# Optimization experiments

Hardware: AMD Instinct MI355X
Metric: run time of the kernel (lower is better)

## Reference

```python
import jax, jax.numpy as jnp
import numpy as np

CX, CY, FX, FY = 334.081, 169.808, 460.585, 460.268
EPS = 1e-07
T_ITER = 1000
MIN_POINTS = 5000
H, W, B = 360, 640, 2


def _point_cloud(depth_img):
    # depth_img: [C,H,W]; channel 2 if C==3 else channel 0
    depth = depth_img[2] if depth_img.shape[0] == 3 else depth_img[0]
    rows, cols = depth.shape
    c = jnp.arange(cols, dtype=depth.dtype)[None, :]
    r = jnp.arange(rows, dtype=depth.dtype)[:, None]
    valid = (depth > 0) & (depth < 65535)
    nanv = jnp.float32(jnp.nan)
    z = jnp.where(valid, depth / 1000.0, nanv)
    x = jnp.where(valid, z * (c - CX) / FX, nanv)
    y = jnp.where(valid, z * (r - CY) / FY, nanv)
    pcd = jnp.stack([x.ravel(), y.ravel(), z.ravel()], axis=1)  # [N,3]
    return pcd, valid.ravel()


def setup_inputs() -> dict:
    key = jax.random.key(0)
    k1, k2 = jax.random.split(key)
    fake = jax.random.uniform(k1, (B, 1, H, W), dtype=jnp.float32)
    real = jax.random.uniform(k2, (B, 1, H, W), dtype=jnp.float32)
    return {"fake": fake, "real": real, "epoch": 5, "show_image": 0}


def _forward(fake, real, epoch):
    real_pcd, vr = _point_cloud(real[0])
    fake_pcd, vf = _point_cloud(fake[0])
    real_pcd = real_pcd * 1000.0
    fake_pcd = fake_pcd * 1000.0
    # pcd[pcd==0] = eps  (NaN==0 is False, NaNs preserved)
    real_pcd = jnp.where(real_pcd == 0, EPS, real_pcd)
    fake_pcd = jnp.where(fake_pcd == 0, EPS, fake_pcd)

    # combined validity mask (real-valid then fake-valid filtering chain)
    m = vr & vf
    cnt = jnp.maximum(jnp.sum(m), 1)

    def sel(v, fill):
        return jnp.where(m, v, fill)

    def mrmse(a, b):
        d = sel(a, 0.0) - sel(b, 0.0)
        return jnp.sqrt(jnp.sum(d * d) / cnt)

    lossX = mrmse(real_pcd[:, 0], fake_pcd[:, 0])
    lossY = mrmse(real_pcd[:, 1], fake_pcd[:, 1])
    lossZ = mrmse(real_pcd[:, 2], fake_pcd[:, 2])
    dlog = jnp.log(jnp.abs(sel(real_pcd[:, 2], 1.0))) - jnp.log(jnp.abs(sel(fake_pcd[:, 2], 1.0)))
    RMSE_log = 10000.0 * jnp.sqrt(jnp.sum(jnp.where(m, dlog * dlog, 0.0)) / cnt)
    loss17 = RMSE_log * jnp.abs(10.0 * (3.0 - jnp.exp(lossX) - jnp.exp(lossY) - jnp.exp(lossZ)))

    # ---- batched RANSAC plane fit on normalized fake cloud ----
    nan_cloud = jnp.where(jnp.isnan(fake_pcd), 0.0, fake_pcd)
    pts = nan_cloud / jnp.max(nan_cloud)  # [N,3]
    N = pts.shape[0]
    thresh = jnp.maximum(jnp.float32(0.025 - 0.001 * epoch), jnp.float32(0.005))

    rkey = jax.random.key(42)
    idx = jax.random.randint(rkey, (T_ITER, 3), 0, N)  # 3 sample points per trial
    p = pts[idx]  # [T,3,3]
    vA = p[:, 1] - p[:, 0]
    vB = p[:, 2] - p[:, 0]
    nrm = jnp.cross(vA, vB)
    nrm = nrm / jnp.linalg.norm(nrm, axis=1, keepdims=True)  # unit normals [T,3]
    kk = -jnp.sum(nrm * p[:, 1], axis=1)  # plane offsets [T]
    dist = pts @ nrm.T + kk[None, :]  # [N,T], |n|=1 so no extra divide
    inl = jnp.abs(dist) <= thresh  # [N,T]
    counts = jnp.sum(inl, axis=0)  # [T]
    # keep first trial with strictly-largest count among counts > minPoints
    score = jnp.where(counts > MIN_POINTS, counts, -1)
    best = jnp.argmax(score)
    a, b, c, d = nrm[best, 0], nrm[best, 1], nrm[best, 2], kk[best]
    inlier_mask = inl[:, best]  # [N]

    # translation/rotation were built via torch.tensor(...) -> detached in torch
    trans = jax.lax.stop_gradient(jnp.stack([jnp.zeros(()), jnp.zeros(()), d / c]))
    n2 = a * a + b * b + c * c
    cos_t = c / jnp.sqrt(n2)
    sin_t = jnp.sqrt((a * a + b * b) / n2)
    sab = jnp.sqrt(a * a + b * b)
    u1 = b / sab
    u2 = -a / sab
    R = jnp.stack([
        jnp.stack([cos_t + u1 * u1 * (1 - cos_t), u1 * u2 * (1 - cos_t), u2 * sin_t]),
        jnp.stack([u1 * u2 * (1 - cos_t), cos_t + u2 * u2 * (1 - cos_t), -u1 * sin_t]),
        jnp.stack([-u2 * sin_t, u1 * sin_t, cos_t]),
    ])
    Rt = jax.lax.stop_gradient(R).T  # torch transposes before matmul

    plane_pts = pts + trans
    zc = (plane_pts @ Rt)[:, 2]  # rotated z for all points; inliers selected by mask
    icnt = jnp.maximum(jnp.sum(inlier_mask), 1)
    zmax = jnp.max(jnp.where(inlier_mask, zc, -jnp.inf))
    zmin = jnp.min(jnp.where(inlier_mask, zc, jnp.inf))
    below = jnp.sum(jnp.where(inlier_mask, jnp.abs(zc - zmax), 0.0)) / icnt
    above = jnp.sum(jnp.where(inlier_mask, jnp.abs(zc - zmin), 0.0)) / icnt
    above = jnp.where(above == 0, jnp.float32(1e-07), above)
    plane_mean_dist_grad = 1000.0 * (above + below)

    loss_curv = loss17 + plane_mean_dist_grad
    delta = jnp.stack([RMSE_log, lossX, lossY, lossZ, plane_mean_dist_grad, loss17])
    return delta, loss_curv


def reference(fake, real, epoch, show_image):
    del show_image  # unused in the loss math
    return _forward(fake, real, epoch)
```

## Files before the change

kernel.cpp:

```cpp
#include <hip/hip_runtime.h>

namespace {

typedef float v2f __attribute__((ext_vector_type(2)));

constexpr int kW = 640;
constexpr unsigned kSpan = 230400u;
constexpr int kB1 = 900;
constexpr int kB3 = 2048;
constexpr int kPPB3 = 225;
constexpr int kB5 = 900;

constexpr size_t kOffMaxv    = 0;
constexpr size_t kOffL17     = 8;
constexpr size_t kOffSel     = 16;
constexpr size_t kOffPlanes  = 512;
constexpr size_t kOffSP      = 512 + 16384;
constexpr size_t kOffZP      = 61440;
constexpr size_t kOffPts     = 2097152;
constexpr size_t kOffPartial = 6291456;

__device__ __forceinline__ unsigned rotl32(unsigned v, int r) {
  return (v << r) | (v >> (32 - r));
}

__device__ __forceinline__ void threefry(unsigned c0, unsigned c1,
                                         unsigned& o0, unsigned& o1) {
  const unsigned ks0 = 0u, ks1 = 42u, ks2 = 0x1BD11BDAu ^ 0u ^ 42u;
  unsigned x0 = c0 + ks0, x1 = c1 + ks1;
#define TFR(r) { x0 += x1; x1 = rotl32(x1, (r)); x1 ^= x0; }
  TFR(13) TFR(15) TFR(26) TFR(6)
  x0 += ks1; x1 += ks2 + 1u;
  TFR(17) TFR(29) TFR(16) TFR(24)
  x0 += ks2; x1 += ks0 + 2u;
  TFR(13) TFR(15) TFR(26) TFR(6)
  x0 += ks0; x1 += ks1 + 3u;
  TFR(17) TFR(29) TFR(16) TFR(24)
  x0 += ks1; x1 += ks2 + 4u;
  TFR(13) TFR(15) TFR(26) TFR(6)
  x0 += ks2; x1 += ks0 + 5u;
#undef TFR
  o0 = x0; o1 = x1;
}

__device__ __forceinline__ void pix_coords(float d, int row, int col, bool& valid,
                                           float& x, float& y, float& z) {
  valid = (d > 0.0f) && (d < 65535.0f);
  float z0 = d / 1000.0f;
  float x0 = z0 * ((float)col - 334.081f) / 460.585f;
  float y0 = z0 * ((float)row - 169.808f) / 460.268f;
  x = x0 * 1000.0f;
  y = y0 * 1000.0f;
  z = z0 * 1000.0f;
  if (x == 0.0f) x = 1e-7f;
  if (y == 0.0f) y = 1e-7f;
  if (z == 0.0f) z = 1e-7f;
}

__device__ __forceinline__ void make_pt(float d, int row, int col, float maxv,
                                        float& x, float& y, float& z) {
  bool v; float a, b, c;
  pix_coords(d, row, col, v, a, b, c);
  x = (v ? a : 0.f) / maxv;
  y = (v ? b : 0.f) / maxv;
  z = (v ? c : 0.f) / maxv;
}

__device__ __forceinline__ float get_thresh(int ep) {
  return (float)fmax(0.025 - 0.001 * (double)ep, 0.005);
}

__global__ __launch_bounds__(256) void k_stats(const float* __restrict__ fake,
                                               const float* __restrict__ real,
                                               char* __restrict__ ws) {
  int* maxvBits = (int*)(ws + kOffMaxv);
  double* sp = (double*)(ws + kOffSP);
  float4* ptsraw = (float4*)(ws + kOffPts);

  const int b = blockIdx.x, t = threadIdx.x;
  const int lane = t & 63, wid = t >> 6;

  __shared__ double sD0[4], sD1[4], sD2[4], sD3[4];
  __shared__ int sI0[4];
  __shared__ float sF0[4];

  int i = b * 256 + t;
  int row = i / kW, col = i - row * kW;
  bool vr, vf; float rx, ry, rz, fx, fy, fz;
  pix_coords(real[i], row, col, vr, rx, ry, rz);
  pix_coords(fake[i], row, col, vf, fx, fy, fz);
  ptsraw[i] = make_float4(vf ? fx : 0.f, vf ? fy : 0.f, vf ? fz : 0.f, 0.f);
  double dx2 = 0, dy2 = 0, dz2 = 0, dl2 = 0; int cc = 0;
  if (vr && vf) {
    float ddx = rx - fx, ddy = ry - fy, ddz = rz - fz;
    dx2 = (double)ddx * (double)ddx;
    dy2 = (double)ddy * (double)ddy;
    dz2 = (double)ddz * (double)ddz;
    double dl = log(fabs((double)rz)) - log(fabs((double)fz));
    dl2 = dl * dl;
    cc = 1;
  }
  float mx = vf ? fmaxf(fmaxf(fx, fy), fz) : 0.0f;
  for (int o = 32; o; o >>= 1) {
    dx2 += __shfl_down(dx2, o); dy2 += __shfl_down(dy2, o);
    dz2 += __shfl_down(dz2, o); dl2 += __shfl_down(dl2, o);
    cc += __shfl_down(cc, o);
    mx = fmaxf(mx, __shfl_down(mx, o));
  }
  if (lane == 0) { sD0[wid]=dx2; sD1[wid]=dy2; sD2[wid]=dz2; sD3[wid]=dl2;
                   sI0[wid]=cc; sF0[wid]=mx; }
  __syncthreads();
  if (t == 0) {
    double* e = sp + (size_t)b * 6;
    e[0] = sD0[0]+sD0[1]+sD0[2]+sD0[3];
    e[1] = sD1[0]+sD1[1]+sD1[2]+sD1[3];
    e[2] = sD2[0]+sD2[1]+sD2[2]+sD2[3];
    e[3] = sD3[0]+sD3[1]+sD3[2]+sD3[3];
    e[4] = (double)(sI0[0]+sI0[1]+sI0[2]+sI0[3]);
    float bm = fmaxf(fmaxf(sF0[0], sF0[1]), fmaxf(sF0[2], sF0[3]));
    atomicMax(maxvBits, (int)__float_as_uint(bm));
  }
}

__global__ __launch_bounds__(256) void k_mid(const float* __restrict__ fake,
                                             float* __restrict__ out,
                                             char* __restrict__ ws) {
  const int* maxvBits = (const int*)(ws + kOffMaxv);
  double* loss17p = (double*)(ws + kOffL17);
  unsigned* selkeyp = (unsigned*)(ws + kOffSel);
  float4* planes = (float4*)(ws + kOffPlanes);
  const double* sp = (const double*)(ws + kOffSP);
  float4* pts = (float4*)(ws + kOffPts);

  const int t = threadIdx.x;
  const int lane = t & 63, wid = t >> 6;

  if (blockIdx.x >= 17) {
    const float maxv = __uint_as_float((unsigned)*maxvBits);
    int i = (blockIdx.x - 17) * 256 + t;
    float4 r = pts[i];
    pts[i] = make_float4(r.x / maxv, r.y / maxv, r.z / maxv, 0.f);
  } else if (blockIdx.x == 16) {
    __shared__ double sD0[4], sD1[4], sD2[4], sD3[4];
    __shared__ int sI0[4];
    double gx = 0, gy = 0, gz = 0, gl = 0; int gc = 0;
    for (int r = t; r < kB1; r += 256) {
      const double* e = sp + (size_t)r * 6;
      gx += e[0]; gy += e[1]; gz += e[2]; gl += e[3];
      gc += (int)e[4];
    }
    for (int o = 32; o; o >>= 1) {
      gx += __shfl_down(gx, o); gy += __shfl_down(gy, o);
      gz += __shfl_down(gz, o); gl += __shfl_down(gl, o);
      gc += __shfl_down(gc, o);
    }
    if (lane == 0) { sD0[wid]=gx; sD1[wid]=gy; sD2[wid]=gz; sD3[wid]=gl; sI0[wid]=gc; }
    __syncthreads();
    if (t == 0) {
      double SX = sD0[0]+sD0[1]+sD0[2]+sD0[3];
      double SY = sD1[0]+sD1[1]+sD1[2]+sD1[3];
      double SZ = sD2[0]+sD2[1]+sD2[2]+sD2[3];
      double SL = sD3[0]+sD3[1]+sD3[2]+sD3[3];
      int CN = sI0[0]+sI0[1]+sI0[2]+sI0[3];
      double cntd = (CN > 0) ? (double)CN : 1.0;
      double lossX = sqrt(SX / cntd);
      double lossY = sqrt(SY / cntd);
      double lossZ = sqrt(SZ / cntd);
      double rmse_log = 10000.0 * sqrt(SL / cntd);
      double loss17 = rmse_log * fabs(10.0 * (3.0 - exp(lossX) - exp(lossY) - exp(lossZ)));
      *loss17p = loss17;
      *selkeyp = 0u;
      out[0] = (float)rmse_log;
      out[1] = (float)lossX;
      out[2] = (float)lossY;
      out[3] = (float)lossZ;
      out[5] = (float)loss17;
    }
  } else {
    const float maxv = __uint_as_float((unsigned)*maxvBits);
    __shared__ float sX[192], sY[192], sZ[192];
    if (t < 192) {
      int j = t / 3;
      int v = t - j * 3;
      int pid = blockIdx.x * 64 + j;
      if (pid < 1000) {
        unsigned p = 3u * (unsigned)pid + (unsigned)v;
        unsigned o0, o1;
        threefry(p, p + 3000u, o0, o1);
        unsigned idx = o1 % kSpan;
        int row = (int)(idx / kW), col = (int)idx - row * kW;
        float x, y, z;
        make_pt(fake[idx], row, col, maxv, x, y, z);
        sX[t] = x; sY[t] = y; sZ[t] = z;
      }
    }
    __syncthreads();
    if (t < 64) {
      int pid = blockIdx.x * 64 + t;
      if (pid < 1000) {
        float px[3], py[3], pz[3];
#pragma unroll
        for (int v = 0; v < 3; v++) {
          px[v] = sX[3 * t + v]; py[v] = sY[3 * t + v]; pz[v] = sZ[3 * t + v];
        }
        float ax = px[1]-px[0], ay = py[1]-py[0], az = pz[1]-pz[0];
        float bx = px[2]-px[0], by = py[2]-py[0], bz = pz[2]-pz[0];
        float nx = ay*bz - az*by;
        float ny = az*bx - ax*bz;
        float nz = ax*by - ay*bx;
        float nn = sqrtf(nx*nx + ny*ny + nz*nz);
        nx /= nn; ny /= nn; nz /= nn;
        float kk = -(nx*px[1] + ny*py[1] + nz*pz[1]);
        planes[pid] = make_float4(nx, ny, nz, kk);
      } else {
        planes[pid] = make_float4(0.f, 0.f, 0.f, 3e38f);
      }
    }
  }
}

__global__ __launch_bounds__(256) void k_count(const int* __restrict__ epoch,
                                               const float4* __restrict__ planes,
                                               const float4* __restrict__ pts,
                                               unsigned* __restrict__ partial) {
  const int b = blockIdx.x, t = threadIdx.x;
  const int pb = b >> 1, ph = b & 1;
  const float th = get_thresh(*epoch);

  int pid = ph * 512 + t * 2;
  float4 p0 = planes[pid + 0], p1 = planes[pid + 1];
  v2f Ax = {p0.x, p1.x}, Ay = {p0.y, p1.y}, Az = {p0.z, p1.z}, Aw = {p0.w, p1.w};

  const float4* __restrict__ base = pts + pb * kPPB3;

  int c0 = 0, c1 = 0;
#pragma unroll 5
  for (int s = 0; s < kPPB3; ++s) {
    float4 q = base[s];
    v2f qx = {q.x, q.x}, qy = {q.y, q.y}, qz = {q.z, q.z};
    v2f dA = __builtin_elementwise_fma(qx, Ax,
             __builtin_elementwise_fma(qy, Ay,
             __builtin_elementwise_fma(qz, Az, Aw)));
    c0 += (fabsf(dA.x) <= th) ? 1 : 0;
    c1 += (fabsf(dA.y) <= th) ? 1 : 0;
  }
  partial[b * 256 + t] = (unsigned)c0 | ((unsigned)c1 << 16);
}

__global__ __launch_bounds__(256) void k_select(char* __restrict__ ws) {
  unsigned* selkeyp = (unsigned*)(ws + kOffSel);
  const unsigned* partial = (const unsigned*)(ws + kOffPartial);

  const int r = blockIdx.x;
  const int t = threadIdx.x;

  __shared__ unsigned sAcc[64][5];

  int l = t & 63;
  int chunk = t >> 6;
  int p = r * 64 + l;
  int ph = p >> 9;
  int to = (p & 511) >> 1;
  int j = p & 1;
  unsigned cnt = 0;
  for (int pb = chunk * 256; pb < chunk * 256 + 256; ++pb) {
    unsigned v = partial[(pb * 2 + ph) * 256 + to];
    cnt += (v >> (16 * j)) & 0xFFFFu;
  }
  sAcc[l][chunk] = cnt;
  __syncthreads();

  unsigned mykey = 0u;
  if (t < 64) {
    unsigned tot = sAcc[t][0] + sAcc[t][1] + sAcc[t][2] + sAcc[t][3];
    int p2 = r * 64 + t;
    if (p2 < 1000) {
      int score = ((int)tot > 5000) ? (int)tot : -1;
      mykey = ((unsigned)(score + 2) << 10) | (unsigned)(1023 - p2);
    }
  }
  for (int o = 32; o; o >>= 1) {
    unsigned other = __shfl_down(mykey, o);
    mykey = other > mykey ? other : mykey;
  }
  if (t == 0) atomicMax(selkeyp, mykey);
}

__global__ __launch_bounds__(256) void k_zc(const int* __restrict__ epoch,
                                            char* __restrict__ ws) {
  const float4* planes = (const float4*)(ws + kOffPlanes);
  unsigned long long* zp = (unsigned long long*)(ws + kOffZP);
  const float4* pts = (const float4*)(ws + kOffPts);

  const int b = blockIdx.x, t = threadIdx.x;
  const int lane = t & 63, wid = t >> 6;
  const float th = get_thresh(*epoch);

  unsigned selkey = *(const unsigned*)(ws + kOffSel);
  int best = 1023 - (int)(selkey & 1023u);
  float4 pl = planes[best];
  const float a = pl.x, bb = pl.y, c = pl.z, d = pl.w;
  float n2 = a * a + bb * bb + c * c;
  float cos_t = c / sqrtf(n2);
  float sin_t = sqrtf((a * a + bb * bb) / n2);
  float sab = sqrtf(a * a + bb * bb);
  float u1 = bb / sab, u2 = -a / sab;
  const float r0 = -u2 * sin_t, r1 = u1 * sin_t, r2 = cos_t, tz = d / c;

  __shared__ double sD0[4];
  __shared__ int sI0[4];
  __shared__ float sF0[4], sF1[4];

  double sz = 0.0; int ic = 0; float zmx = -INFINITY, zmn = -INFINITY;
  {
    float4 q = pts[b * 256 + t];
    float dist = fmaf(q.x, a, fmaf(q.y, bb, fmaf(q.z, c, d)));
    if (fabsf(dist) <= th) {
      float zc = fmaf(q.x, r0, fmaf(q.y, r1, (q.z + tz) * r2));
      sz = (double)zc; ic = 1; zmx = zc; zmn = -zc;
    }
  }
  for (int o = 32; o; o >>= 1) {
    sz += __shfl_down(sz, o); ic += __shfl_down(ic, o);
    zmx = fmaxf(zmx, __shfl_down(zmx, o));
    zmn = fmaxf(zmn, __shfl_down(zmn, o));
  }
  if (lane == 0) { sD0[wid] = sz; sI0[wid] = ic; sF0[wid] = zmx; sF1[wid] = zmn; }
  __syncthreads();
  if (t == 0) {
    unsigned long long* e = zp + (size_t)b * 4;
    e[0] = __double_as_longlong(sD0[0]+sD0[1]+sD0[2]+sD0[3]);
    e[1] = (unsigned long long)(sI0[0]+sI0[1]+sI0[2]+sI0[3]);
    float bmx = fmaxf(fmaxf(sF0[0], sF0[1]), fmaxf(sF0[2], sF0[3]));
    float bmn = fmaxf(fmaxf(sF1[0], sF1[1]), fmaxf(sF1[2], sF1[3]));
    e[2] = (unsigned long long)__float_as_uint(bmx) |
           ((unsigned long long)__float_as_uint(bmn) << 32);
  }
}

__global__ __launch_bounds__(256) void k_final(float* __restrict__ out,
                                               char* __restrict__ ws) {
  const double* loss17p = (const double*)(ws + kOffL17);
  const unsigned long long* zp = (const unsigned long long*)(ws + kOffZP);

  const int t = threadIdx.x;
  const int lane = t & 63, wid = t >> 6;

  __shared__ double sD0[4];
  __shared__ int sI0[4];
  __shared__ float sF0[4], sF1[4];

  double gs = 0.0; int gi = 0; float gmx = -INFINITY, gmn = -INFINITY;
  for (int r = t; r < kB5; r += 256) {
    const unsigned long long* e = zp + (size_t)r * 4;
    gs += __longlong_as_double(e[0]);
    gi += (int)e[1];
    unsigned long long mm = e[2];
    gmx = fmaxf(gmx, __uint_as_float((unsigned)(mm & 0xFFFFFFFFu)));
    gmn = fmaxf(gmn, __uint_as_float((unsigned)(mm >> 32)));
  }
  for (int o = 32; o; o >>= 1) {
    gs += __shfl_down(gs, o); gi += __shfl_down(gi, o);
    gmx = fmaxf(gmx, __shfl_down(gmx, o));
    gmn = fmaxf(gmn, __shfl_down(gmn, o));
  }
  if (lane == 0) { sD0[wid] = gs; sI0[wid] = gi; sF0[wid] = gmx; sF1[wid] = gmn; }
  __syncthreads();
  if (t == 0) {
    double S = sD0[0]+sD0[1]+sD0[2]+sD0[3];
    int IC = sI0[0]+sI0[1]+sI0[2]+sI0[3];
    float MX = fmaxf(fmaxf(sF0[0], sF0[1]), fmaxf(sF0[2], sF0[3]));
    float MN = fmaxf(fmaxf(sF1[0], sF1[1]), fmaxf(sF1[2], sF1[3]));
    double below = 0.0, above = 0.0;
    if (IC > 0) {
      double icd = (double)IC;
      double mean = S / icd;
      below = (double)MX - mean;
      above = mean - (double)(-MN);
    }
    if (above == 0.0) above = 1e-7;
    double pmdg = 1000.0 * (above + below);
    out[4] = (float)pmdg;
    out[6] = (float)(*loss17p + pmdg);
  }
}

}

extern "C" void kernel_launch(void* const* d_in, const int* in_sizes, int n_in,
                              void* d_out, int out_size, void* d_ws, size_t ws_size,
                              hipStream_t stream) {
  (void)in_sizes; (void)n_in; (void)out_size; (void)ws_size;
  const float* fake = (const float*)d_in[0];
  const float* real = (const float*)d_in[1];
  const int* epoch = (const int*)d_in[2];
  float* out = (float*)d_out;
  char* ws = (char*)d_ws;

  const float4* planes = (const float4*)(ws + kOffPlanes);
  const float4* pts    = (const float4*)(ws + kOffPts);
  unsigned* partial    = (unsigned*)(ws + kOffPartial);

  k_stats<<<kB1, 256, 0, stream>>>(fake, real, ws);
  k_mid<<<917, 256, 0, stream>>>(fake, out, ws);
  k_count<<<kB3, 256, 0, stream>>>(epoch, planes, pts, partial);
  k_select<<<16, 256, 0, stream>>>(ws);
  k_zc<<<kB5, 256, 0, stream>>>(epoch, ws);
  k_final<<<1, 256, 0, stream>>>(out, ws);
}
```

Measured before the change: 135.9 us.

## Evaluate eight planes per thread in RANSAC inlier counting with byte-packed partials

```diff
diff --git a/kernel.cpp b/kernel.cpp
--- a/kernel.cpp
+++ b/kernel.cpp
@@ -7,7 +7,7 @@
 constexpr int kW = 640;
 constexpr unsigned kSpan = 230400u;
 constexpr int kB1 = 900;
-constexpr int kB3 = 2048;
+constexpr int kB3 = 1024;
 constexpr int kPPB3 = 225;
 constexpr int kB5 = 900;
 
@@ -219,21 +219,25 @@
   }
 }
 
-__global__ __launch_bounds__(256) void k_count(const int* __restrict__ epoch,
+__global__ __launch_bounds__(128) void k_count(const int* __restrict__ epoch,
                                                const float4* __restrict__ planes,
                                                const float4* __restrict__ pts,
-                                               unsigned* __restrict__ partial) {
+                                               uint2* __restrict__ partial) {
   const int b = blockIdx.x, t = threadIdx.x;
-  const int pb = b >> 1, ph = b & 1;
   const float th = get_thresh(*epoch);
 
-  int pid = ph * 512 + t * 2;
-  float4 p0 = planes[pid + 0], p1 = planes[pid + 1];
+  float4 p0 = planes[t * 8 + 0], p1 = planes[t * 8 + 1];
+  float4 p2 = planes[t * 8 + 2], p3 = planes[t * 8 + 3];
+  float4 p4 = planes[t * 8 + 4], p5 = planes[t * 8 + 5];
+  float4 p6 = planes[t * 8 + 6], p7 = planes[t * 8 + 7];
   v2f Ax = {p0.x, p1.x}, Ay = {p0.y, p1.y}, Az = {p0.z, p1.z}, Aw = {p0.w, p1.w};
-
-  const float4* __restrict__ base = pts + pb * kPPB3;
-
-  int c0 = 0, c1 = 0;
+  v2f Bx = {p2.x, p3.x}, By = {p2.y, p3.y}, Bz = {p2.z, p3.z}, Bw = {p2.w, p3.w};
+  v2f Cx = {p4.x, p5.x}, Cy = {p4.y, p5.y}, Cz = {p4.z, p5.z}, Cw = {p4.w, p5.w};
+  v2f Dx = {p6.x, p7.x}, Dy = {p6.y, p7.y}, Dz = {p6.z, p7.z}, Dw = {p6.w, p7.w};
+
+  const float4* __restrict__ base = pts + b * kPPB3;
+
+  int c0 = 0, c1 = 0, c2 = 0, c3 = 0, c4 = 0, c5 = 0, c6 = 0, c7 = 0;
 #pragma unroll 5
   for (int s = 0; s < kPPB3; ++s) {
     float4 q = base[s];
@@ -241,10 +245,27 @@
     v2f dA = __builtin_elementwise_fma(qx, Ax,
              __builtin_elementwise_fma(qy, Ay,
              __builtin_elementwise_fma(qz, Az, Aw)));
+    v2f dB = __builtin_elementwise_fma(qx, Bx,
+             __builtin_elementwise_fma(qy, By,
+             __builtin_elementwise_fma(qz, Bz, Bw)));
+    v2f dC = __builtin_elementwise_fma(qx, Cx,
+             __builtin_elementwise_fma(qy, Cy,
+             __builtin_elementwise_fma(qz, Cz, Cw)));
+    v2f dD = __builtin_elementwise_fma(qx, Dx,
+             __builtin_elementwise_fma(qy, Dy,
+             __builtin_elementwise_fma(qz, Dz, Dw)));
     c0 += (fabsf(dA.x) <= th) ? 1 : 0;
     c1 += (fabsf(dA.y) <= th) ? 1 : 0;
-  }
-  partial[b * 256 + t] = (unsigned)c0 | ((unsigned)c1 << 16);
+    c2 += (fabsf(dB.x) <= th) ? 1 : 0;
+    c3 += (fabsf(dB.y) <= th) ? 1 : 0;
+    c4 += (fabsf(dC.x) <= th) ? 1 : 0;
+    c5 += (fabsf(dC.y) <= th) ? 1 : 0;
+    c6 += (fabsf(dD.x) <= th) ? 1 : 0;
+    c7 += (fabsf(dD.y) <= th) ? 1 : 0;
+  }
+  partial[b * 128 + t] = make_uint2(
+      (unsigned)c0 | ((unsigned)c1 << 8) | ((unsigned)c2 << 16) | ((unsigned)c3 << 24),
+      (unsigned)c4 | ((unsigned)c5 << 8) | ((unsigned)c6 << 16) | ((unsigned)c7 << 24));
 }
 
 __global__ __launch_bounds__(256) void k_select(char* __restrict__ ws) {
@@ -259,13 +280,13 @@
   int l = t & 63;
   int chunk = t >> 6;
   int p = r * 64 + l;
-  int ph = p >> 9;
-  int to = (p & 511) >> 1;
-  int j = p & 1;
+  int to = p >> 3;
+  int w = (p & 7) >> 2;
+  int byt = p & 3;
   unsigned cnt = 0;
   for (int pb = chunk * 256; pb < chunk * 256 + 256; ++pb) {
-    unsigned v = partial[(pb * 2 + ph) * 256 + to];
-    cnt += (v >> (16 * j)) & 0xFFFFu;
+    unsigned v = partial[(pb * 128 + to) * 2 + w];
+    cnt += (v >> (8 * byt)) & 0xFFu;
   }
   sAcc[l][chunk] = cnt;
   __syncthreads();
@@ -399,11 +420,11 @@
 
   const float4* planes = (const float4*)(ws + kOffPlanes);
   const float4* pts    = (const float4*)(ws + kOffPts);
-  unsigned* partial    = (unsigned*)(ws + kOffPartial);
+  uint2* partial       = (uint2*)(ws + kOffPartial);
 
   k_stats<<<kB1, 256, 0, stream>>>(fake, real, ws);
   k_mid<<<917, 256, 0, stream>>>(fake, out, ws);
-  k_count<<<kB3, 256, 0, stream>>>(epoch, planes, pts, partial);
+  k_count<<<kB3, 128, 0, stream>>>(epoch, planes, pts, partial);
   k_select<<<16, 256, 0, stream>>>(ws);
   k_zc<<<kB5, 256, 0, stream>>>(epoch, ws);
   k_final<<<1, 256, 0, stream>>>(out, ws);
```

Result: no change. 134.7 us (-0.9%).
